# Kernel tuning notes

Hardware: AMD Instinct MI355X
Metric: run time of the kernel (lower is better)

The kernel has to match this reference:

```python
import jax, jax.numpy as jnp
import numpy as np

B, N_IN, N_OUT, C = 4, 512, 1024, 64
INIT_LENGTH_SCALE = 0.1


def setup_inputs() -> dict:
    key = jax.random.key(0)
    k1, k2, k3, k4, k5 = jax.random.split(key, 5)
    x = jax.random.uniform(k1, (B, N_IN, 1), dtype=jnp.float32)
    y = jax.random.normal(k2, (B, N_IN, C), dtype=jnp.float32)
    t = jax.random.uniform(k3, (B, N_OUT, 1), dtype=jnp.float32)
    # learnable params: per-channel log length-scale, pointwise linear C -> 1
    sigma = jnp.full((C,), np.log(INIT_LENGTH_SCALE), dtype=jnp.float32)
    w = jax.random.normal(k4, (C, 1), dtype=jnp.float32) / np.sqrt(C)
    b = jnp.zeros((1,), dtype=jnp.float32)
    return {"x": x, "y": y, "t": t, "sigma": sigma, "w": w, "b": b}


def reference(x, y, t, sigma, w, b):
    # pairwise squared distances: (B, n_in, n_out)
    dists = (x - jnp.swapaxes(t, 1, 2)) ** 2
    scales = jnp.exp(sigma)  # (C,)
    # RBF weights, broadcast over channels: (B, n_in, n_out, C)
    wt = jnp.exp(-0.5 * dists[..., None] / scales**2)
    # weighted sum over input points: (B, n_out, C)
    y_out = jnp.einsum("bnc,bnmc->bmc", y, wt)
    # pointwise linear C -> 1: (B, n_out, 1)
    return y_out @ w + b
```

## Files before the change

### kernel.cpp

```cpp
#include <hip/hip_runtime.h>

constexpr int Bb   = 4;
constexpr int NIN  = 512;
constexpr int NOUT = 1024;
constexpr int CC   = 64;

constexpr int MTILE = 64;
constexpr int NGRP  = 4;
constexpr int NPER  = NIN / NGRP;

__global__ __launch_bounds__(256) void rbf_prep(
    const float* __restrict__ y, const float* __restrict__ w,
    float* __restrict__ ytil)
{
    const int lane = threadIdx.x & 63;
    const int i    = blockIdx.x * 4 + (threadIdx.x >> 6);
    float v = y[(size_t)i * CC + lane] * w[lane];
#pragma unroll
    for (int off = 32; off > 0; off >>= 1) v += __shfl_xor(v, off, 64);
    if (lane == 0) ytil[i] = v;
}

__global__ __launch_bounds__(256) void rbf_main(
    const float* __restrict__ x,     const float* __restrict__ y,
    const float* __restrict__ t,     const float* __restrict__ sigma,
    const float* __restrict__ w,     const float* __restrict__ bias,
    const float* __restrict__ ytil,  float* __restrict__ out)
{
    __shared__ float part[NGRP * MTILE];
    const int tid  = threadIdx.x;
    const int lane = tid & 63;
    const int g    = tid >> 6;
    const int mt   = blockIdx.x & 15;
    const int b    = blockIdx.x >> 4;
    const int m    = mt * MTILE + lane;

    const float s0  = sigma[0];
    const bool  uni = (__ballot(sigma[lane] == s0) == ~0ull);

    if (uni) {
        const float s  = 0.84932180f * __expf(-s0);
        const float tm = t[b * NOUT + m] * s;
        const float* __restrict__ xb = x    + b * NIN + g * NPER;
        const float* __restrict__ yb = ytil + b * NIN + g * NPER;
        float a0 = 0.f, a1 = 0.f, a2 = 0.f, a3 = 0.f;
#pragma unroll 8
        for (int n = 0; n < NPER; n += 4) {
            const float d0 = xb[n + 0] * s - tm;
            const float d1 = xb[n + 1] * s - tm;
            const float d2 = xb[n + 2] * s - tm;
            const float d3 = xb[n + 3] * s - tm;
            a0 += __builtin_amdgcn_exp2f(-(d0 * d0)) * yb[n + 0];
            a1 += __builtin_amdgcn_exp2f(-(d1 * d1)) * yb[n + 1];
            a2 += __builtin_amdgcn_exp2f(-(d2 * d2)) * yb[n + 2];
            a3 += __builtin_amdgcn_exp2f(-(d3 * d3)) * yb[n + 3];
        }
        part[tid] = (a0 + a1) + (a2 + a3);
        __syncthreads();
        if (g == 0) {
            const float r = (part[lane] + part[64 + lane]) +
                            (part[128 + lane] + part[192 + lane]) + bias[0];
            out[b * NOUT + m] = r;
        }
    } else {
        const float kc2 = -0.72134752f * __expf(-2.0f * sigma[lane]);
        const float wc  = w[lane];
        const float* __restrict__ xb = x + b * NIN;
        const float* __restrict__ yb = y + (size_t)b * NIN * CC + lane;
        for (int j = 0; j < 16; ++j) {
            const int   mm = mt * MTILE + g * 16 + j;
            const float tm = t[b * NOUT + mm];
            float acc = 0.f;
            for (int n = 0; n < NIN; ++n) {
                const float d = xb[n] - tm;
                acc += __builtin_amdgcn_exp2f(d * d * kc2) * yb[(size_t)n * CC];
            }
            float p = acc * wc;
#pragma unroll
            for (int off = 32; off > 0; off >>= 1) p += __shfl_xor(p, off, 64);
            if (lane == 0) out[b * NOUT + mm] = p + bias[0];
        }
    }
}

extern "C" void kernel_launch(void* const* d_in, const int* in_sizes, int n_in,
                              void* d_out, int out_size, void* d_ws, size_t ws_size,
                              hipStream_t stream) {
    const float* x     = (const float*)d_in[0];
    const float* y     = (const float*)d_in[1];
    const float* t     = (const float*)d_in[2];
    const float* sigma = (const float*)d_in[3];
    const float* w     = (const float*)d_in[4];
    const float* bias  = (const float*)d_in[5];
    float* out  = (float*)d_out;
    float* ytil = (float*)d_ws;

    rbf_prep<<<Bb * NIN / 4, 256, 0, stream>>>(y, w, ytil);
    rbf_main<<<Bb * (NOUT / MTILE), 256, 0, stream>>>(x, y, t, sigma, w, bias, ytil, out);
}
```

Before: 67.41 us.

## Fuse y·w projection into main RBF kernel with LDS staging and smaller tiles

Removes the separate prep kernel. Each block now recomputes the per-batch y·w projection for all 512 inputs into shared memory and pre-scales x there too. The output tile shrinks to 16 points with 16 input groups and a shuffle-plus-LDS reduction, which raises the grid to 256 blocks. This saves one launch and the global round-trip of the projection. In exchange, every one of the 64 blocks per batch re-reads that batch's full 128KB of y.

```diff
diff --git a/kernel.cpp b/kernel.cpp
--- a/kernel.cpp
+++ b/kernel.cpp
@@ -5,70 +5,83 @@
 constexpr int NOUT = 1024;
 constexpr int CC   = 64;
 
-constexpr int MTILE = 64;
-constexpr int NGRP  = 4;
+constexpr int MTILE = 16;
+constexpr int NGRP  = 16;
 constexpr int NPER  = NIN / NGRP;
+constexpr int MBLKS = NOUT / MTILE;
 
-__global__ __launch_bounds__(256) void rbf_prep(
-    const float* __restrict__ y, const float* __restrict__ w,
-    float* __restrict__ ytil)
-{
-    const int lane = threadIdx.x & 63;
-    const int i    = blockIdx.x * 4 + (threadIdx.x >> 6);
-    float v = y[(size_t)i * CC + lane] * w[lane];
-#pragma unroll
-    for (int off = 32; off > 0; off >>= 1) v += __shfl_xor(v, off, 64);
-    if (lane == 0) ytil[i] = v;
-}
-
-__global__ __launch_bounds__(256) void rbf_main(
+__global__ __launch_bounds__(256) void rbf_fused(
     const float* __restrict__ x,     const float* __restrict__ y,
     const float* __restrict__ t,     const float* __restrict__ sigma,
     const float* __restrict__ w,     const float* __restrict__ bias,
-    const float* __restrict__ ytil,  float* __restrict__ out)
+    float* __restrict__ out)
 {
-    __shared__ float part[NGRP * MTILE];
+    __shared__ float ytil_s[NIN];
+    __shared__ float xs_s[NIN];
+    __shared__ float red[64];
+
     const int tid  = threadIdx.x;
     const int lane = tid & 63;
-    const int g    = tid >> 6;
-    const int mt   = blockIdx.x & 15;
-    const int b    = blockIdx.x >> 4;
-    const int m    = mt * MTILE + lane;
+    const int wv   = tid >> 6;
+    const int mt   = blockIdx.x & (MBLKS - 1);
+    const int b    = blockIdx.x >> 6;
 
     const float s0  = sigma[0];
     const bool  uni = (__ballot(sigma[lane] == s0) == ~0ull);
 
     if (uni) {
-        const float s  = 0.84932180f * __expf(-s0);
-        const float tm = t[b * NOUT + m] * s;
-        const float* __restrict__ xb = x    + b * NIN + g * NPER;
-        const float* __restrict__ yb = ytil + b * NIN + g * NPER;
+        const float s = 0.84932180f * __expf(-s0);
+
+        const float4* __restrict__ w4 = (const float4*)w;
+#pragma unroll
+        for (int r = 0; r < 2; ++r) {
+            const int n = r * 256 + tid;
+            const float4* __restrict__ y4 = (const float4*)(y + ((size_t)b * NIN + n) * CC);
+            float acc = 0.f;
+#pragma unroll
+            for (int j = 0; j < 16; ++j) {
+                const float4 a = y4[j], ww = w4[j];
+                acc += a.x * ww.x + a.y * ww.y + a.z * ww.z + a.w * ww.w;
+            }
+            ytil_s[n] = acc;
+            xs_s[n]   = x[b * NIN + n] * s;
+        }
+        __syncthreads();
+
+        const int   ml = tid & (MTILE - 1);
+        const int   g  = tid >> 4;
+        const float tm = t[b * NOUT + mt * MTILE + ml] * s;
+        const float* __restrict__ xp = xs_s   + g * NPER;
+        const float* __restrict__ yp = ytil_s + g * NPER;
         float a0 = 0.f, a1 = 0.f, a2 = 0.f, a3 = 0.f;
-#pragma unroll 8
+#pragma unroll
         for (int n = 0; n < NPER; n += 4) {
-            const float d0 = xb[n + 0] * s - tm;
-            const float d1 = xb[n + 1] * s - tm;
-            const float d2 = xb[n + 2] * s - tm;
-            const float d3 = xb[n + 3] * s - tm;
-            a0 += __builtin_amdgcn_exp2f(-(d0 * d0)) * yb[n + 0];
-            a1 += __builtin_amdgcn_exp2f(-(d1 * d1)) * yb[n + 1];
-            a2 += __builtin_amdgcn_exp2f(-(d2 * d2)) * yb[n + 2];
-            a3 += __builtin_amdgcn_exp2f(-(d3 * d3)) * yb[n + 3];
+            const float d0 = xp[n + 0] - tm;
+            const float d1 = xp[n + 1] - tm;
+            const float d2 = xp[n + 2] - tm;
+            const float d3 = xp[n + 3] - tm;
+            a0 += __builtin_amdgcn_exp2f(-(d0 * d0)) * yp[n + 0];
+            a1 += __builtin_amdgcn_exp2f(-(d1 * d1)) * yp[n + 1];
+            a2 += __builtin_amdgcn_exp2f(-(d2 * d2)) * yp[n + 2];
+            a3 += __builtin_amdgcn_exp2f(-(d3 * d3)) * yp[n + 3];
         }
-        part[tid] = (a0 + a1) + (a2 + a3);
+        float p = (a0 + a1) + (a2 + a3);
+        p += __shfl_xor(p, 16, 64);
+        p += __shfl_xor(p, 32, 64);
+        if (lane < 16) red[wv * 16 + lane] = p;
         __syncthreads();
-        if (g == 0) {
-            const float r = (part[lane] + part[64 + lane]) +
-                            (part[128 + lane] + part[192 + lane]) + bias[0];
-            out[b * NOUT + m] = r;
+        if (tid < 16) {
+            const float r = (red[tid] + red[16 + tid]) +
+                            (red[32 + tid] + red[48 + tid]) + bias[0];
+            out[b * NOUT + mt * MTILE + tid] = r;
         }
     } else {
         const float kc2 = -0.72134752f * __expf(-2.0f * sigma[lane]);
         const float wc  = w[lane];
         const float* __restrict__ xb = x + b * NIN;
         const float* __restrict__ yb = y + (size_t)b * NIN * CC + lane;
-        for (int j = 0; j < 16; ++j) {
-            const int   mm = mt * MTILE + g * 16 + j;
+        for (int j = 0; j < 4; ++j) {
+            const int   mm = mt * MTILE + wv * 4 + j;
             const float tm = t[b * NOUT + mm];
             float acc = 0.f;
             for (int n = 0; n < NIN; ++n) {
@@ -92,9 +105,7 @@
     const float* sigma = (const float*)d_in[3];
     const float* w     = (const float*)d_in[4];
     const float* bias  = (const float*)d_in[5];
-    float* out  = (float*)d_out;
-    float* ytil = (float*)d_ws;
+    float* out = (float*)d_out;
 
-    rbf_prep<<<Bb * NIN / 4, 256, 0, stream>>>(y, w, ytil);
-    rbf_main<<<Bb * (NOUT / MTILE), 256, 0, stream>>>(x, y, t, sigma, w, bias, ytil, out);
+    rbf_fused<<<Bb * MBLKS, 256, 0, stream>>>(x, y, t, sigma, w, bias, out);
 }
```

Result: no change. 68.50 us (+1.6%).
